# Performance work log

Measured on AMD Instinct MI355X. Metric: run time of the kernel, lower is better.

The kernel has to match this reference:

```python
import jax, jax.numpy as jnp
import numpy as np

NUM_GRAPHS = 10000
N_NODES = 1000000
FEAT = 128

def setup_inputs() -> dict:
    key = jax.random.key(0)
    k1, k2 = jax.random.split(key)
    h_t = jax.random.normal(k1, (N_NODES, FEAT), dtype=jnp.float32)
    batch = jnp.sort(jax.random.randint(k2, (N_NODES,), 0, NUM_GRAPHS, dtype=jnp.int64))
    return {"h_t": h_t, "batch": batch}

def reference(h_t, batch):
    # The original shuffles node features *within* each graph before sum-pooling.
    # Sum pooling is permutation-invariant, so the per-graph randperm shuffle is a
    # no-op mathematically: output == segment_sum(h_t, batch).
    # This fuses the whole per-graph loop into a single scatter-add.
    return jax.ops.segment_sum(h_t, batch, num_segments=NUM_GRAPHS)
```

## Files before the change

### kernel.cpp

```cpp
#include <hip/hip_runtime.h>


#define FEAT 128
#define ROWS_PER_WAVE 128

typedef float vfloat4 __attribute__((ext_vector_type(4)));

static __device__ inline vfloat4 ntload4(const float* p) {
  return __builtin_nontemporal_load((const vfloat4*)p);
}

__global__ __launch_bounds__(256) void segsum_kernel(
    const float* __restrict__ h,
    const int* __restrict__ batch,
    float* __restrict__ out,
    int n_rows) {
  const int wave = (blockIdx.x * blockDim.x + threadIdx.x) >> 6;
  const int lane = threadIdx.x & 63;
  const int sub = lane >> 5;
  const int col = (lane & 31) * 4;

  long long row0 = (long long)wave * ROWS_PER_WAVE;
  if (row0 >= n_rows) return;
  long long row_end = row0 + ROWS_PER_WAVE;
  if (row_end > n_rows) row_end = n_rows;

  vfloat4 acc = {0.0f, 0.0f, 0.0f, 0.0f};
  long long first = row0 + sub;
  int cur = batch[first < n_rows ? first : (n_rows - 1)];

#define STEP(B, V)                                        \
  {                                                       \
    const int b_ = (B);                                   \
    if (b_ != cur) {          \
      float* dst = out + (long long)cur * FEAT + col;     \
      atomicAdd(dst + 0, acc.x);                          \
      atomicAdd(dst + 1, acc.y);                          \
      atomicAdd(dst + 2, acc.z);                          \
      atomicAdd(dst + 3, acc.w);                          \
      acc.x = 0.0f; acc.y = 0.0f;                         \
      acc.z = 0.0f; acc.w = 0.0f;                         \
      cur = b_;                                           \
    }                                                     \
    acc.x += (V).x; acc.y += (V).y;                       \
    acc.z += (V).z; acc.w += (V).w;                       \
  }

  long long r = row0;
  for (; r + 16 <= row_end; r += 16) {
    const int4 ba = *(const int4*)(batch + r);
    const int4 bb = *(const int4*)(batch + r + 4);
    const int4 bc = *(const int4*)(batch + r + 8);
    const int4 bd = *(const int4*)(batch + r + 12);
    const float* hp = h + (r + sub) * (long long)FEAT + col;
    vfloat4 v0 = ntload4(hp + 0 * 2 * FEAT);
    vfloat4 v1 = ntload4(hp + 1 * 2 * FEAT);
    vfloat4 v2 = ntload4(hp + 2 * 2 * FEAT);
    vfloat4 v3 = ntload4(hp + 3 * 2 * FEAT);
    vfloat4 v4 = ntload4(hp + 4 * 2 * FEAT);
    vfloat4 v5 = ntload4(hp + 5 * 2 * FEAT);
    vfloat4 v6 = ntload4(hp + 6 * 2 * FEAT);
    vfloat4 v7 = ntload4(hp + 7 * 2 * FEAT);

    STEP(sub ? ba.y : ba.x, v0)
    STEP(sub ? ba.w : ba.z, v1)
    STEP(sub ? bb.y : bb.x, v2)
    STEP(sub ? bb.w : bb.z, v3)
    STEP(sub ? bc.y : bc.x, v4)
    STEP(sub ? bc.w : bc.z, v5)
    STEP(sub ? bd.y : bd.x, v6)
    STEP(sub ? bd.w : bd.z, v7)
  }

  for (; r + 2 <= row_end; r += 2) {
    const int b = batch[r + sub];
    const vfloat4 v = *(const vfloat4*)(h + (r + sub) * (long long)FEAT + col);
    STEP(b, v)
  }
  if (r < row_end && sub == 0) {
    const int b = batch[r];
    const vfloat4 v = *(const vfloat4*)(h + r * (long long)FEAT + col);
    STEP(b, v)
  }
#undef STEP

  {
    float* dst = out + (long long)cur * FEAT + col;
    atomicAdd(dst + 0, acc.x);
    atomicAdd(dst + 1, acc.y);
    atomicAdd(dst + 2, acc.z);
    atomicAdd(dst + 3, acc.w);
  }
}

extern "C" void kernel_launch(void* const* d_in, const int* in_sizes, int n_in,
                              void* d_out, int out_size, void* d_ws, size_t ws_size,
                              hipStream_t stream) {
  const float* h_t = (const float*)d_in[0];
  const int* batch = (const int*)d_in[1];
  float* out = (float*)d_out;
  const int n_rows = in_sizes[1];

  hipMemsetAsync(d_out, 0, (size_t)out_size * sizeof(float), stream);

  const int n_waves = (n_rows + ROWS_PER_WAVE - 1) / ROWS_PER_WAVE;
  const int block = 256;
  const int waves_per_block = block / 64;
  const int grid = (n_waves + waves_per_block - 1) / waves_per_block;

  segsum_kernel<<<grid, block, 0, stream>>>(h_t, batch, out, n_rows);
}
```

Baseline: 638.0 us.

## Double-buffer row loads in segment-sum loop and drop nontemporal loads

Restructures the main loop into a two-stage software pipeline: the next 16-row chunk of features and batch ids is loaded into a second register set while the current chunk is accumulated. This aims to hide global memory latency behind the compare/atomic work. It also replaces the nontemporal vector loads with ordinary loads. The cost is higher register pressure, which may reduce occupancy.

After: 653.6 us. +2.4%, slower.

```diff
diff --git a/kernel.cpp b/kernel.cpp
--- a/kernel.cpp
+++ b/kernel.cpp
@@ -5,10 +5,6 @@
 #define ROWS_PER_WAVE 128
 
 typedef float vfloat4 __attribute__((ext_vector_type(4)));
-
-static __device__ inline vfloat4 ntload4(const float* p) {
-  return __builtin_nontemporal_load((const vfloat4*)p);
-}
 
 __global__ __launch_bounds__(256) void segsum_kernel(
     const float* __restrict__ h,
@@ -46,30 +42,63 @@
     acc.z += (V).z; acc.w += (V).w;                       \
   }
 
+  int4 baA, bbA, bcA, bdA, baB, bbB, bcB, bdB;
+  vfloat4 v0A, v1A, v2A, v3A, v4A, v5A, v6A, v7A;
+  vfloat4 v0B, v1B, v2B, v3B, v4B, v5B, v6B, v7B;
+
+  const int* bcur = batch + row0;
+  const float* hcur = h + (row0 + sub) * (long long)FEAT + col;
   long long r = row0;
-  for (; r + 16 <= row_end; r += 16) {
-    const int4 ba = *(const int4*)(batch + r);
-    const int4 bb = *(const int4*)(batch + r + 4);
-    const int4 bc = *(const int4*)(batch + r + 8);
-    const int4 bd = *(const int4*)(batch + r + 12);
-    const float* hp = h + (r + sub) * (long long)FEAT + col;
-    vfloat4 v0 = ntload4(hp + 0 * 2 * FEAT);
-    vfloat4 v1 = ntload4(hp + 1 * 2 * FEAT);
-    vfloat4 v2 = ntload4(hp + 2 * 2 * FEAT);
-    vfloat4 v3 = ntload4(hp + 3 * 2 * FEAT);
-    vfloat4 v4 = ntload4(hp + 4 * 2 * FEAT);
-    vfloat4 v5 = ntload4(hp + 5 * 2 * FEAT);
-    vfloat4 v6 = ntload4(hp + 6 * 2 * FEAT);
-    vfloat4 v7 = ntload4(hp + 7 * 2 * FEAT);
 
-    STEP(sub ? ba.y : ba.x, v0)
-    STEP(sub ? ba.w : ba.z, v1)
-    STEP(sub ? bb.y : bb.x, v2)
-    STEP(sub ? bb.w : bb.z, v3)
-    STEP(sub ? bc.y : bc.x, v4)
-    STEP(sub ? bc.w : bc.z, v5)
-    STEP(sub ? bd.y : bd.x, v6)
-    STEP(sub ? bd.w : bd.z, v7)
+#define LOAD_STAGE(S)                                     \
+  {                                                       \
+    ba##S = *(const int4*)(bcur + 0);                     \
+    bb##S = *(const int4*)(bcur + 4);                     \
+    bc##S = *(const int4*)(bcur + 8);                     \
+    bd##S = *(const int4*)(bcur + 12);                    \
+    v0##S = *(const vfloat4*)(hcur + 0 * 2 * FEAT);       \
+    v1##S = *(const vfloat4*)(hcur + 1 * 2 * FEAT);       \
+    v2##S = *(const vfloat4*)(hcur + 2 * 2 * FEAT);       \
+    v3##S = *(const vfloat4*)(hcur + 3 * 2 * FEAT);       \
+    v4##S = *(const vfloat4*)(hcur + 4 * 2 * FEAT);       \
+    v5##S = *(const vfloat4*)(hcur + 5 * 2 * FEAT);       \
+    v6##S = *(const vfloat4*)(hcur + 6 * 2 * FEAT);       \
+    v7##S = *(const vfloat4*)(hcur + 7 * 2 * FEAT);       \
+    bcur += 16;                                           \
+    hcur += 16 * FEAT;                                    \
+    r += 16;                                              \
+  }
+
+#define CONSUME_STAGE(S)                                  \
+  {                                                       \
+    STEP(sub ? ba##S.y : ba##S.x, v0##S)                  \
+    STEP(sub ? ba##S.w : ba##S.z, v1##S)                  \
+    STEP(sub ? bb##S.y : bb##S.x, v2##S)                  \
+    STEP(sub ? bb##S.w : bb##S.z, v3##S)                  \
+    STEP(sub ? bc##S.y : bc##S.x, v4##S)                  \
+    STEP(sub ? bc##S.w : bc##S.z, v5##S)                  \
+    STEP(sub ? bd##S.y : bd##S.x, v6##S)                  \
+    STEP(sub ? bd##S.w : bd##S.z, v7##S)                  \
+  }
+
+  if (r + 16 <= row_end) {
+    LOAD_STAGE(A)
+    for (;;) {
+      if (r + 16 <= row_end) {
+        LOAD_STAGE(B)
+        CONSUME_STAGE(A)
+      } else {
+        CONSUME_STAGE(A)
+        break;
+      }
+      if (r + 16 <= row_end) {
+        LOAD_STAGE(A)
+        CONSUME_STAGE(B)
+      } else {
+        CONSUME_STAGE(B)
+        break;
+      }
+    }
   }
 
   for (; r + 2 <= row_end; r += 2) {
@@ -83,6 +112,8 @@
     STEP(b, v)
   }
 #undef STEP
+#undef LOAD_STAGE
+#undef CONSUME_STAGE
 
   {
     float* dst = out + (long long)cur * FEAT + col;
```

## Stage batch indices in LDS and add a wave-uniform fast path for 8-row blocks

Applied to the files above, without the earlier changes.

Each wave preloads its 128 batch indices into shared memory once, instead of loading int4 vectors from global memory inside the loop. The main loop now handles 8 rows per iteration instead of 16, with 4 vector loads per lane. A wave-wide __all check takes a branch-free summation path when every row in the block belongs to the same segment. The change also adds a launch-bounds occupancy hint (8) and uses nontemporal loads in the tail loops. It trades fewer in-flight loads per iteration for less divergence and less index-load overhead.

Result: no change. 643.5 us (+0.9%).

```diff
diff --git a/kernel.cpp b/kernel.cpp
--- a/kernel.cpp
+++ b/kernel.cpp
@@ -10,11 +10,13 @@
   return __builtin_nontemporal_load((const vfloat4*)p);
 }
 
-__global__ __launch_bounds__(256) void segsum_kernel(
+__global__ __launch_bounds__(256, 8) void segsum_kernel(
     const float* __restrict__ h,
     const int* __restrict__ batch,
     float* __restrict__ out,
     int n_rows) {
+  __shared__ int bl[4 * ROWS_PER_WAVE];
+  const int wid = threadIdx.x >> 6;
   const int wave = (blockIdx.x * blockDim.x + threadIdx.x) >> 6;
   const int lane = threadIdx.x & 63;
   const int sub = lane >> 5;
@@ -25,15 +27,26 @@
   long long row_end = row0 + ROWS_PER_WAVE;
   if (row_end > n_rows) row_end = n_rows;
 
+  int* myb = bl + wid * ROWS_PER_WAVE;
+  {
+    long long i0 = row0 + lane;
+    long long i1 = row0 + 64 + lane;
+    const long long last = (long long)n_rows - 1;
+    if (i0 > last) i0 = last;
+    if (i1 > last) i1 = last;
+    myb[lane] = batch[i0];
+    myb[lane + 64] = batch[i1];
+  }
+
   vfloat4 acc = {0.0f, 0.0f, 0.0f, 0.0f};
-  long long first = row0 + sub;
-  int cur = batch[first < n_rows ? first : (n_rows - 1)];
+  int cur = myb[sub];
+  float* const outc = out + col;
 
 #define STEP(B, V)                                        \
   {                                                       \
     const int b_ = (B);                                   \
     if (b_ != cur) {          \
-      float* dst = out + (long long)cur * FEAT + col;     \
+      float* dst = outc + (long long)cur * FEAT;          \
       atomicAdd(dst + 0, acc.x);                          \
       atomicAdd(dst + 1, acc.y);                          \
       atomicAdd(dst + 2, acc.z);                          \
@@ -46,46 +59,62 @@
     acc.z += (V).z; acc.w += (V).w;                       \
   }
 
+  const float* hp = h + (row0 + sub) * (long long)FEAT + col;
+  int li = sub;
   long long r = row0;
-  for (; r + 16 <= row_end; r += 16) {
-    const int4 ba = *(const int4*)(batch + r);
-    const int4 bb = *(const int4*)(batch + r + 4);
-    const int4 bc = *(const int4*)(batch + r + 8);
-    const int4 bd = *(const int4*)(batch + r + 12);
-    const float* hp = h + (r + sub) * (long long)FEAT + col;
+  const long long nblk = (row_end - row0) >> 3;
+
+  for (long long blk = 0; blk < nblk; ++blk) {
     vfloat4 v0 = ntload4(hp + 0 * 2 * FEAT);
     vfloat4 v1 = ntload4(hp + 1 * 2 * FEAT);
     vfloat4 v2 = ntload4(hp + 2 * 2 * FEAT);
     vfloat4 v3 = ntload4(hp + 3 * 2 * FEAT);
-    vfloat4 v4 = ntload4(hp + 4 * 2 * FEAT);
-    vfloat4 v5 = ntload4(hp + 5 * 2 * FEAT);
-    vfloat4 v6 = ntload4(hp + 6 * 2 * FEAT);
-    vfloat4 v7 = ntload4(hp + 7 * 2 * FEAT);
+    const int b0 = myb[li + 0];
+    const int b1 = myb[li + 2];
+    const int b2 = myb[li + 4];
+    const int b3 = myb[li + 6];
 
-    STEP(sub ? ba.y : ba.x, v0)
-    STEP(sub ? ba.w : ba.z, v1)
-    STEP(sub ? bb.y : bb.x, v2)
-    STEP(sub ? bb.w : bb.z, v3)
-    STEP(sub ? bc.y : bc.x, v4)
-    STEP(sub ? bc.w : bc.z, v5)
-    STEP(sub ? bd.y : bd.x, v6)
-    STEP(sub ? bd.w : bd.z, v7)
+    if (__all(b0 == b3)) {
+      if (b0 != cur) {
+        float* dst = outc + (long long)cur * FEAT;
+        atomicAdd(dst + 0, acc.x);
+        atomicAdd(dst + 1, acc.y);
+        atomicAdd(dst + 2, acc.z);
+        atomicAdd(dst + 3, acc.w);
+        acc.x = 0.0f; acc.y = 0.0f; acc.z = 0.0f; acc.w = 0.0f;
+        cur = b0;
+      }
+      acc.x += v0.x + v1.x + v2.x + v3.x;
+      acc.y += v0.y + v1.y + v2.y + v3.y;
+      acc.z += v0.z + v1.z + v2.z + v3.z;
+      acc.w += v0.w + v1.w + v2.w + v3.w;
+    } else {
+      STEP(b0, v0)
+      STEP(b1, v1)
+      STEP(b2, v2)
+      STEP(b3, v3)
+    }
+    hp += 8 * FEAT;
+    li += 8;
+    r += 8;
   }
 
   for (; r + 2 <= row_end; r += 2) {
-    const int b = batch[r + sub];
-    const vfloat4 v = *(const vfloat4*)(h + (r + sub) * (long long)FEAT + col);
+    const int b = myb[li];
+    const vfloat4 v = ntload4(hp);
     STEP(b, v)
+    hp += 2 * FEAT;
+    li += 2;
   }
   if (r < row_end && sub == 0) {
-    const int b = batch[r];
-    const vfloat4 v = *(const vfloat4*)(h + r * (long long)FEAT + col);
+    const int b = myb[li];
+    const vfloat4 v = ntload4(hp);
     STEP(b, v)
   }
 #undef STEP
 
   {
-    float* dst = out + (long long)cur * FEAT + col;
+    float* dst = outc + (long long)cur * FEAT;
     atomicAdd(dst + 0, acc.x);
     atomicAdd(dst + 1, acc.y);
     atomicAdd(dst + 2, acc.z);
```
